# Optimization experiments

Measured on AMD Instinct MI355X. Metric: run time of the kernel, lower is better.

Reference implementation:

```python
import jax, jax.numpy as jnp
import numpy as np

N_NODES = 30000
N_EDGES = 480000
NFEAT = 256
HEADS = 4
C0 = 64      # layer0 out_channels
C1 = 40      # layer1 out_channels = nclass
NEG_SLOPE = 0.2
EPS = 1e-16


def glorot(key, shape, fan):
    # PyG glorot: uniform(-s, s), s = sqrt(6/(fan_in+fan_out)) over last 2 dims
    s = float(np.sqrt(6.0 / fan))
    return jax.random.uniform(key, shape, jnp.float32, -s, s)


def setup_inputs() -> dict:
    key = jax.random.key(0)
    ks = jax.random.split(key, 10)
    x = jax.random.normal(ks[0], (N_NODES, NFEAT), jnp.float32)
    src = jax.random.randint(ks[1], (N_EDGES,), 0, N_NODES)
    off = jax.random.randint(ks[2], (N_EDGES,), 1, N_NODES)
    dst = (src + off) % N_NODES  # guaranteed no self loops
    edge_index = jnp.stack([src, dst]).astype(jnp.int64)
    # layer 0 params (in=256 -> heads*out = 4*64, concat=True)
    w0 = glorot(ks[3], (NFEAT, HEADS * C0), NFEAT + HEADS * C0)
    att0 = glorot(ks[4], (1, HEADS, 2 * C0), HEADS + 2 * C0)
    b0 = jnp.zeros((HEADS * C0,), jnp.float32)
    # layer 1 params (in=256 -> heads*out = 4*40, concat=False)
    w1 = glorot(ks[5], (HEADS * C0, HEADS * C1), HEADS * C0 + HEADS * C1)
    att1 = glorot(ks[6], (1, HEADS, 2 * C1), HEADS + 2 * C1)
    b1 = jnp.zeros((C1,), jnp.float32)
    return {"x": x, "edge_index": edge_index, "w0": w0, "att0": att0,
            "b0": b0, "w1": w1, "att1": att1, "b1": b1}


def geo_layer(x, row, col, W, att, bias, heads, out_ch, concat):
    n = x.shape[0]
    h = (x @ W).reshape(n, heads, out_ch)          # [N,H,C]
    x_i = h[row]                                   # [E,H,C] gather (target per old-PyG i=0)
    x_j = h[col]                                   # [E,H,C]
    # 'gat' attention: leaky_relu(sum(cat(x_i,x_j) * att))
    a_l = att[:, :, :out_ch]
    a_r = att[:, :, out_ch:]
    alpha = jnp.sum(x_i * a_l, -1) + jnp.sum(x_j * a_r, -1)   # [E,H]
    alpha = jax.nn.leaky_relu(alpha, NEG_SLOPE)
    # segment softmax over target node (row)
    amax = jax.ops.segment_max(alpha, row, num_segments=n)
    ex = jnp.exp(alpha - amax[row])
    denom = jax.ops.segment_sum(ex, row, num_segments=n)
    alpha = ex / (denom[row] + EPS)
    neighbor = x_j * alpha[..., None]              # [E,H,C]
    out = jax.ops.segment_sum(neighbor, row, num_segments=n)  # [N,H,C]
    if concat:
        out = out.reshape(n, heads * out_ch)
    else:
        out = out.mean(axis=1)
    return out + bias


def reference(x, edge_index, w0, att0, b0, w1, att1, b1):
    n = x.shape[0]
    loops = jnp.arange(n, dtype=edge_index.dtype)
    row = jnp.concatenate([edge_index[0], loops])
    col = jnp.concatenate([edge_index[1], loops])
    out = geo_layer(x, row, col, w0, att0, b0, HEADS, C0, True)
    out = jax.nn.relu(out)
    out = geo_layer(out, row, col, w1, att1, b1, HEADS, C1, False)
    return out  # [N, nclass]
```

## Files before the change

### kernel.cpp

```cpp
#include <hip/hip_runtime.h>
#include <math.h>

#define N_NODES 30000
#define N_EDGESN 480000
#define NFEAT 256
#define HEADS 4
#define C0V 64
#define C1V 40
#define HC0 (HEADS*C0V)
#define HC1 (HEADS*C1V)
#define NEG_SLOPE 0.2f
#define EPSV 1e-16f

typedef unsigned short ushort_t;
typedef __attribute__((ext_vector_type(8))) short short8v;
typedef __attribute__((ext_vector_type(4))) float f32x4;

__device__ __forceinline__ float lrelu(float x) { return x >= 0.f ? x : x * NEG_SLOPE; }

__device__ __forceinline__ float b2f(unsigned int u16) {
  union { unsigned int u; float f; } v; v.u = u16 << 16; return v.f;
}
__device__ __forceinline__ float b2f_lo(unsigned int u) {
  union { unsigned int u; float f; } v; v.u = u << 16; return v.f;
}
__device__ __forceinline__ float b2f_hi(unsigned int u) {
  union { unsigned int u; float f; } v; v.u = u & 0xffff0000u; return v.f;
}
__device__ __forceinline__ unsigned short f2b(float f) {
  union { float f; unsigned int u; } v; v.f = f;
  unsigned int u = v.u + 0x7FFFu + ((v.u >> 16) & 1u);
  return (unsigned short)(u >> 16);
}

__global__ __launch_bounds__(256) void wtrans_both(const float* __restrict__ W0,
    const float* __restrict__ W1, ushort_t* __restrict__ W0t,
    ushort_t* __restrict__ W1t) {
  const int idx = blockIdx.x * 256 + threadIdx.x;
  constexpr int T0 = NFEAT * HC0;
  constexpr int T1 = HC0 * HC1;
  if (idx < T0) {
    const int k = idx / HC0, nf = idx - k * HC0;
    W0t[(size_t)nf * NFEAT + k] = f2b(W0[idx]);
  } else if (idx < T0 + T1) {
    const int i2 = idx - T0;
    const int k = i2 / HC1, nf = i2 - k * HC1;
    W1t[(size_t)nf * HC0 + k] = f2b(W1[i2]);
  }
}

#define KDIM 256
#define KPAD 264
template <int NFW, int CG, int NSTRIP, bool A_F32, int FUSE>
__global__ __launch_bounds__(256) void gemm_mfma2(const void* __restrict__ Ap,
    const ushort_t* __restrict__ Wt, ushort_t* __restrict__ C, int M,
    const float* __restrict__ att, float* __restrict__ al, float* __restrict__ ar) {
  __shared__ ushort_t As[NSTRIP][16][KPAD];
  const int tid = threadIdx.x;
  const int row_base = blockIdx.x * (NSTRIP * 16);
  constexpr int CHUNKS = NSTRIP * 16 * (KDIM / 8);
  for (int c = tid; c < CHUNKS; c += 256) {
    const int r = c / (KDIM / 8);
    const int ko = (c - r * (KDIM / 8)) * 8;
    const int s = r >> 4, rr = r & 15;
    uint4 w = make_uint4(0u, 0u, 0u, 0u);
    if (row_base + r < M) {
      if (A_F32) {
        const float* A = (const float*)Ap + (size_t)(row_base + r) * KDIM + ko;
        const float4 lo = *reinterpret_cast<const float4*>(A);
        const float4 hi = *reinterpret_cast<const float4*>(A + 4);
        w.x = (unsigned)f2b(lo.x) | ((unsigned)f2b(lo.y) << 16);
        w.y = (unsigned)f2b(lo.z) | ((unsigned)f2b(lo.w) << 16);
        w.z = (unsigned)f2b(hi.x) | ((unsigned)f2b(hi.y) << 16);
        w.w = (unsigned)f2b(hi.z) | ((unsigned)f2b(hi.w) << 16);
      } else {
        w = *reinterpret_cast<const uint4*>(
            (const ushort_t*)Ap + (size_t)(row_base + r) * KDIM + ko);
      }
    }
    *reinterpret_cast<uint4*>(&As[s][rr][ko]) = w;
  }
  __syncthreads();

  const int wid = tid >> 6, lane = tid & 63;
  const int s = wid / CG, cg = wid - s * CG;
  const int r_a = lane & 15, kg = lane >> 4;
  const int row0 = row_base + s * 16;
  constexpr int N = CG * NFW * 16;

  f32x4 acc[NFW];
#pragma unroll
  for (int f = 0; f < NFW; ++f) acc[f] = (f32x4){0.f, 0.f, 0.f, 0.f};

#pragma unroll
  for (int k0 = 0; k0 < KDIM; k0 += 32) {
    const short8v a = *reinterpret_cast<const short8v*>(&As[s][r_a][k0 + kg * 8]);
#pragma unroll
    for (int f = 0; f < NFW; ++f) {
      const short8v b = *reinterpret_cast<const short8v*>(
          Wt + (size_t)((cg * NFW + f) * 16 + r_a) * KDIM + k0 + kg * 8);
      acc[f] = __builtin_amdgcn_mfma_f32_16x16x32_bf16(a, b, acc[f], 0, 0, 0);
    }
  }
  if (row0 >= M) return;
#pragma unroll
  for (int f = 0; f < NFW; ++f) {
#pragma unroll
    for (int r = 0; r < 4; ++r) {
      C[(size_t)(row0 + kg * 4 + r) * N + (cg * NFW + f) * 16 + r_a] = f2b(acc[f][r]);
    }
  }
  if (FUSE == 1) {
    float hpl[4] = {0.f, 0.f, 0.f, 0.f}, hpr[4] = {0.f, 0.f, 0.f, 0.f};
#pragma unroll
    for (int f = 0; f < NFW; ++f) {
      const int cc = f * 16 + r_a;
      const float wlv = att[cg * 128 + cc];
      const float wrv = att[cg * 128 + 64 + cc];
#pragma unroll
      for (int r = 0; r < 4; ++r) {
        hpl[r] = fmaf(acc[f][r], wlv, hpl[r]);
        hpr[r] = fmaf(acc[f][r], wrv, hpr[r]);
      }
    }
#pragma unroll
    for (int o = 1; o < 16; o <<= 1) {
#pragma unroll
      for (int r = 0; r < 4; ++r) {
        hpl[r] += __shfl_xor(hpl[r], o);
        hpr[r] += __shfl_xor(hpr[r], o);
      }
    }
    if (r_a == 0) {
#pragma unroll
      for (int r = 0; r < 4; ++r) {
        const int row = row0 + kg * 4 + r;
        al[(size_t)row * 4 + cg] = hpl[r];
        ar[(size_t)row * 4 + cg] = hpr[r];
      }
    }
  } else if (FUSE == 2) {
    float hpa[4] = {0,0,0,0}, hpb[4] = {0,0,0,0};
    float hra[4] = {0,0,0,0}, hrb[4] = {0,0,0,0};
#pragma unroll
    for (int f = 0; f < NFW; ++f) {
      const int col = cg * 80 + f * 16 + r_a;
      const int hd = col / 40;
      const int cc = col - hd * 40;
      const float wlv = att[hd * 80 + cc];
      const float wrv = att[hd * 80 + 40 + cc];
      const bool isB = (hd & 1);
#pragma unroll
      for (int r = 0; r < 4; ++r) {
        const float v = acc[f][r];
        if (isB) { hpb[r] = fmaf(v, wlv, hpb[r]); hrb[r] = fmaf(v, wrv, hrb[r]); }
        else     { hpa[r] = fmaf(v, wlv, hpa[r]); hra[r] = fmaf(v, wrv, hra[r]); }
      }
    }
#pragma unroll
    for (int o = 1; o < 16; o <<= 1) {
#pragma unroll
      for (int r = 0; r < 4; ++r) {
        hpa[r] += __shfl_xor(hpa[r], o); hpb[r] += __shfl_xor(hpb[r], o);
        hra[r] += __shfl_xor(hra[r], o); hrb[r] += __shfl_xor(hrb[r], o);
      }
    }
    if (r_a == 0) {
#pragma unroll
      for (int r = 0; r < 4; ++r) {
        const int row = row0 + kg * 4 + r;
        al[(size_t)row * 4 + cg * 2 + 0] = hpa[r];
        al[(size_t)row * 4 + cg * 2 + 1] = hpb[r];
        ar[(size_t)row * 4 + cg * 2 + 0] = hra[r];
        ar[(size_t)row * 4 + cg * 2 + 1] = hrb[r];
      }
    }
  }
}

__global__ void hist_kernel(const int* __restrict__ src, int* __restrict__ deg, int E) {
  const int e = blockIdx.x * blockDim.x + threadIdx.x;
  if (e < E) atomicAdd(&deg[src[e]], 1);
}

__global__ __launch_bounds__(1024) void scan_kernel(const int* __restrict__ deg,
    int* __restrict__ rowstart, int n) {
  __shared__ int carry;
  __shared__ int wsum[16];
  const int tid = threadIdx.x;
  const int lane = tid & 63, w = tid >> 6;
  if (tid == 0) { carry = 0; rowstart[0] = 0; }
  __syncthreads();
  for (int base = 0; base < n; base += 1024) {
    const int idx = base + tid;
    int x = (idx < n) ? deg[idx] : 0;
#pragma unroll
    for (int o = 1; o < 64; o <<= 1) { int y = __shfl_up(x, o); if (lane >= o) x += y; }
    if (lane == 63) wsum[w] = x;
    __syncthreads();
    if (w == 0) {
      int s = (lane < 16) ? wsum[lane] : 0;
#pragma unroll
      for (int o = 1; o < 16; o <<= 1) { int y = __shfl_up(s, o); if (lane >= o) s += y; }
      if (lane < 16) wsum[lane] = s;
    }
    __syncthreads();
    const int add = (w > 0 ? wsum[w - 1] : 0) + carry;
    if (idx < n) rowstart[idx + 1] = x + add;
    __syncthreads();
    if (tid == 0) carry += wsum[15];
    __syncthreads();
  }
}

__global__ void scatter_kernel(const int* __restrict__ src, const int* __restrict__ dst,
    const int* __restrict__ rowstart, int* __restrict__ fill, int* __restrict__ scol,
    int E) {
  const int e = blockIdx.x * blockDim.x + threadIdx.x;
  if (e < E) {
    const int r = src[e];
    const int pos = rowstart[r] + atomicAdd(&fill[r], 1);
    scol[pos] = dst[e];
  }
}

template <int C, bool CONCAT_RELU>
__global__ __launch_bounds__(256) void gat_agg6(const ushort_t* __restrict__ h,
    const float* __restrict__ al, const float* __restrict__ ar,
    const int* __restrict__ rowstart, const int* __restrict__ scol,
    const float* __restrict__ bias, void* __restrict__ outv, int n) {
  constexpr int ROW = HEADS * C;
  constexpr int LPG = ROW / 8;
  constexpr int NG  = 64 / LPG;
  constexpr int EMAX = N_EDGESN - 1;
  __shared__ float smA[CONCAT_RELU ? 1 : 4][CONCAT_RELU ? 1 : NG]
                      [CONCAT_RELU ? 1 : ROW];
  __shared__ float smT[CONCAT_RELU ? 1 : 4][CONCAT_RELU ? 1 : NG * LPG];
  const int wid = threadIdx.x >> 6, lane = threadIdx.x & 63;
  const int i = blockIdx.x * 4 + wid;
  if (i >= n) return;
  const int s0 = rowstart[i], s1 = rowstart[i + 1];

  const float4 al4 = *reinterpret_cast<const float4*>(al + (size_t)i * 4);
  const float4 ari = *reinterpret_cast<const float4*>(ar + (size_t)i * 4);
  const float es0 = __expf(lrelu(al4.x + ari.x));
  const float es1 = __expf(lrelu(al4.y + ari.y));
  const float es2 = __expf(lrelu(al4.z + ari.z));
  const float es3 = __expf(lrelu(al4.w + ari.w));

  const int g  = lane / LPG;
  const int cl = lane - g * LPG;
  const bool act = g < NG;
  const int hd = (cl * 8) / C;
  const float al_h = hd < 2 ? (hd == 0 ? al4.x : al4.y) : (hd == 2 ? al4.z : al4.w);
  const float es_h = hd < 2 ? (hd == 0 ? es0 : es1) : (hd == 2 ? es2 : es3);

  float t = 0.f;
  float acc[8];
#pragma unroll
  for (int k = 0; k < 8; ++k) acc[k] = 0.f;

  if (g == 0) {
    const uint4 hv = *reinterpret_cast<const uint4*>(h + (size_t)i * ROW + cl * 8);
    acc[0] = es_h * b2f_lo(hv.x); acc[1] = es_h * b2f_hi(hv.x);
    acc[2] = es_h * b2f_lo(hv.y); acc[3] = es_h * b2f_hi(hv.y);
    acc[4] = es_h * b2f_lo(hv.z); acc[5] = es_h * b2f_hi(hv.z);
    acc[6] = es_h * b2f_lo(hv.w); acc[7] = es_h * b2f_hi(hv.w);
  }

#define FMA8(W, HV) \
  acc[0] = fmaf(W, b2f_lo(HV.x), acc[0]); acc[1] = fmaf(W, b2f_hi(HV.x), acc[1]); \
  acc[2] = fmaf(W, b2f_lo(HV.y), acc[2]); acc[3] = fmaf(W, b2f_hi(HV.y), acc[3]); \
  acc[4] = fmaf(W, b2f_lo(HV.z), acc[4]); acc[5] = fmaf(W, b2f_hi(HV.z), acc[5]); \
  acc[6] = fmaf(W, b2f_lo(HV.w), acc[6]); acc[7] = fmaf(W, b2f_hi(HV.w), acc[7])

  if (act) {
    int e = s0 + g;
    int ja = scol[min(e, EMAX)];
    int jb = scol[min(e + NG, EMAX)];
    for (; e + NG < s1; e += 2 * NG) {
      const int jc = scol[min(e + 2 * NG, EMAX)];
      const int jd = scol[min(e + 3 * NG, EMAX)];
      const float ara = ar[(size_t)ja * 4 + hd];
      const float arb = ar[(size_t)jb * 4 + hd];
      const uint4 ha = *reinterpret_cast<const uint4*>(h + (size_t)ja * ROW + cl * 8);
      const uint4 hb = *reinterpret_cast<const uint4*>(h + (size_t)jb * ROW + cl * 8);
      const float wa = __expf(lrelu(al_h + ara));
      const float wb = __expf(lrelu(al_h + arb));
      t += wa + wb;
      FMA8(wa, ha); FMA8(wb, hb);
      ja = jc; jb = jd;
    }
    if (e < s1) {
      const float ara = ar[(size_t)ja * 4 + hd];
      const uint4 ha = *reinterpret_cast<const uint4*>(h + (size_t)ja * ROW + cl * 8);
      const float wa = __expf(lrelu(al_h + ara));
      t += wa;
      FMA8(wa, ha);
    }
  }
#undef FMA8

  if (CONCAT_RELU) {
    t += __shfl_xor(t, 32);
    const float inv = 1.f / (t + es_h + EPSV);
#pragma unroll
    for (int k = 0; k < 8; ++k) acc[k] *= inv;
#pragma unroll
    for (int k = 0; k < 8; ++k) acc[k] += __shfl_xor(acc[k], 32);
    if (g == 0) {
      const float4 blo = *reinterpret_cast<const float4*>(bias + cl * 8);
      const float4 bhi = *reinterpret_cast<const float4*>(bias + cl * 8 + 4);
      uint4 st;
      st.x = (unsigned)f2b(fmaxf(acc[0] + blo.x, 0.f)) |
             ((unsigned)f2b(fmaxf(acc[1] + blo.y, 0.f)) << 16);
      st.y = (unsigned)f2b(fmaxf(acc[2] + blo.z, 0.f)) |
             ((unsigned)f2b(fmaxf(acc[3] + blo.w, 0.f)) << 16);
      st.z = (unsigned)f2b(fmaxf(acc[4] + bhi.x, 0.f)) |
             ((unsigned)f2b(fmaxf(acc[5] + bhi.y, 0.f)) << 16);
      st.w = (unsigned)f2b(fmaxf(acc[6] + bhi.z, 0.f)) |
             ((unsigned)f2b(fmaxf(acc[7] + bhi.w, 0.f)) << 16);
      *reinterpret_cast<uint4*>((ushort_t*)outv + (size_t)i * ROW + cl * 8) = st;
    }
  } else {
    if (act) {
#pragma unroll
      for (int k = 0; k < 8; ++k) smA[wid][g][cl * 8 + k] = acc[k];
      smT[wid][g * LPG + cl] = t;
    }
    __syncthreads();
    if (lane < C) {
      const float es[4] = {es0, es1, es2, es3};
      float s = 0.f;
#pragma unroll
      for (int hh = 0; hh < HEADS; ++hh) {
        float den = es[hh];
#pragma unroll
        for (int gg = 0; gg < NG; ++gg)
          den += smT[wid][gg * LPG + hh * 5];
        float chan = 0.f;
#pragma unroll
        for (int gg = 0; gg < NG; ++gg) chan += smA[wid][gg][hh * C + lane];
        s += chan / (den + EPSV);
      }
      ((float*)outv)[(size_t)i * C + lane] = s * 0.25f + bias[lane];
    }
  }
}

extern "C" void kernel_launch(void* const* d_in, const int* in_sizes, int n_in,
                              void* d_out, int out_size, void* d_ws, size_t ws_size,
                              hipStream_t stream) {
  const float* x    = (const float*)d_in[0];
  const int*   ei   = (const int*)d_in[1];
  const float* w0   = (const float*)d_in[2];
  const float* att0 = (const float*)d_in[3];
  const float* b0   = (const float*)d_in[4];
  const float* w1   = (const float*)d_in[5];
  const float* att1 = (const float*)d_in[6];
  const float* b1   = (const float*)d_in[7];
  float* out = (float*)d_out;

  char* ws = (char*)d_ws;
  size_t off = 0;
  auto alloc = [&](size_t bytes) -> void* {
    void* p = ws + off;
    off += (bytes + 255) & ~(size_t)255;
    return p;
  };
  ushort_t* h0b = (ushort_t*)alloc((size_t)N_NODES * HC0 * 2);
  ushort_t* o0b = (ushort_t*)alloc((size_t)N_NODES * HC0 * 2);
  float* al0 = (float*)alloc((size_t)N_NODES * HEADS * 4);
  float* ar0 = (float*)alloc((size_t)N_NODES * HEADS * 4);
  ushort_t* w0t = (ushort_t*)alloc((size_t)HC0 * NFEAT * 2);
  ushort_t* w1t = (ushort_t*)alloc((size_t)HC1 * HC0 * 2);
  int* deg      = (int*)alloc((size_t)N_NODES * 4);
  int* fill     = (int*)alloc((size_t)N_NODES * 4);
  int* rowstart = (int*)alloc((size_t)(N_NODES + 1) * 4);
  int* scol     = (int*)alloc((size_t)N_EDGESN * 4);
  ushort_t* h1b = h0b;
  float* al1 = al0;
  float* ar1 = ar0;

  const int* srcp = ei;
  const int* dstp = ei + N_EDGESN;

  const size_t zlen = (size_t)((char*)fill - (char*)deg) + (size_t)N_NODES * 4;
  hipMemsetAsync(deg, 0, zlen, stream);
  hist_kernel<<<(N_EDGESN + 255) / 256, 256, 0, stream>>>(srcp, deg, N_EDGESN);
  scan_kernel<<<1, 1024, 0, stream>>>(deg, rowstart, N_NODES);
  scatter_kernel<<<(N_EDGESN + 255) / 256, 256, 0, stream>>>(srcp, dstp, rowstart,
                                                             fill, scol, N_EDGESN);
  wtrans_both<<<(NFEAT * HC0 + HC0 * HC1 + 255) / 256, 256, 0, stream>>>(
      w0, w1, w0t, w1t);

  gemm_mfma2<4, 4, 1, true, 1><<<N_NODES / 16, 256, 0, stream>>>(
      x, w0t, h0b, N_NODES, att0, al0, ar0);
  gat_agg6<C0V, true><<<(N_NODES + 3) / 4, 256, 0, stream>>>(
      h0b, al0, ar0, rowstart, scol, b0, o0b, N_NODES);
  gemm_mfma2<5, 2, 2, false, 2><<<(N_NODES + 31) / 32, 256, 0, stream>>>(
      o0b, w1t, h1b, N_NODES, att1, al1, ar1);
  gat_agg6<C1V, false><<<(N_NODES + 3) / 4, 256, 0, stream>>>(
      h1b, al1, ar1, rowstart, scol, b1, out, N_NODES);
}
```

Baseline: 213.9 us.

## Make GEMMs persistent with register-resident weights and double-buffered A strips

Both dense projections become persistent kernels: each wave loads its slice of the transposed bf16 weight matrix into registers once, then loops over 16-row strips with a grid-stride step. The next strip's activations are prefetched into registers and written to a second LDS buffer while the current strip runs MFMAs, so global latency can overlap compute. The memset is replaced by a small zero kernel. The cost is much higher register pressure from holding weights (8×NFW short8 vectors per lane), which may reduce occupancy, plus fewer blocks per launch.

```diff
diff --git a/kernel.cpp b/kernel.cpp
--- a/kernel.cpp
+++ b/kernel.cpp
@@ -11,6 +11,8 @@
 #define HC1 (HEADS*C1V)
 #define NEG_SLOPE 0.2f
 #define EPSV 1e-16f
+#define KDIM 256
+#define KPAD 264
 
 typedef unsigned short ushort_t;
 typedef __attribute__((ext_vector_type(8))) short short8v;
@@ -18,9 +20,6 @@
 
 __device__ __forceinline__ float lrelu(float x) { return x >= 0.f ? x : x * NEG_SLOPE; }
 
-__device__ __forceinline__ float b2f(unsigned int u16) {
-  union { unsigned int u; float f; } v; v.u = u16 << 16; return v.f;
-}
 __device__ __forceinline__ float b2f_lo(unsigned int u) {
   union { unsigned int u; float f; } v; v.u = u << 16; return v.f;
 }
@@ -31,6 +30,11 @@
   union { float f; unsigned int u; } v; v.f = f;
   unsigned int u = v.u + 0x7FFFu + ((v.u >> 16) & 1u);
   return (unsigned short)(u >> 16);
+}
+
+__global__ __launch_bounds__(256) void zero_kernel(int* __restrict__ p, int n) {
+  const int i = blockIdx.x * 256 + threadIdx.x;
+  if (i < n) p[i] = 0;
 }
 
 __global__ __launch_bounds__(256) void wtrans_both(const float* __restrict__ W0,
@@ -49,133 +53,161 @@
   }
 }
 
-#define KDIM 256
-#define KPAD 264
-template <int NFW, int CG, int NSTRIP, bool A_F32, int FUSE>
-__global__ __launch_bounds__(256) void gemm_mfma2(const void* __restrict__ Ap,
-    const ushort_t* __restrict__ Wt, ushort_t* __restrict__ C, int M,
+template <int NFW, int CG, bool A_F32, int FUSE, int NT>
+__global__ __launch_bounds__(NT) void gemm_mfma3(const void* __restrict__ Ap,
+    const ushort_t* __restrict__ Wt, ushort_t* __restrict__ C, int nblk,
     const float* __restrict__ att, float* __restrict__ al, float* __restrict__ ar) {
-  __shared__ ushort_t As[NSTRIP][16][KPAD];
+  constexpr int S = N_NODES / 16;
+  constexpr int N = CG * NFW * 16;
+  constexpr int NCH = 16 * (KDIM / 8) / NT;
+  __shared__ ushort_t As[2][16][KPAD];
   const int tid = threadIdx.x;
-  const int row_base = blockIdx.x * (NSTRIP * 16);
-  constexpr int CHUNKS = NSTRIP * 16 * (KDIM / 8);
-  for (int c = tid; c < CHUNKS; c += 256) {
-    const int r = c / (KDIM / 8);
-    const int ko = (c - r * (KDIM / 8)) * 8;
-    const int s = r >> 4, rr = r & 15;
-    uint4 w = make_uint4(0u, 0u, 0u, 0u);
-    if (row_base + r < M) {
-      if (A_F32) {
-        const float* A = (const float*)Ap + (size_t)(row_base + r) * KDIM + ko;
-        const float4 lo = *reinterpret_cast<const float4*>(A);
-        const float4 hi = *reinterpret_cast<const float4*>(A + 4);
-        w.x = (unsigned)f2b(lo.x) | ((unsigned)f2b(lo.y) << 16);
-        w.y = (unsigned)f2b(lo.z) | ((unsigned)f2b(lo.w) << 16);
-        w.z = (unsigned)f2b(hi.x) | ((unsigned)f2b(hi.y) << 16);
-        w.w = (unsigned)f2b(hi.z) | ((unsigned)f2b(hi.w) << 16);
-      } else {
-        w = *reinterpret_cast<const uint4*>(
-            (const ushort_t*)Ap + (size_t)(row_base + r) * KDIM + ko);
-      }
-    }
-    *reinterpret_cast<uint4*>(&As[s][rr][ko]) = w;
+  const int lane = tid & 63, cg = tid >> 6;
+  const int r_a = lane & 15, kg = lane >> 4;
+
+  short8v B[8][NFW];
+#pragma unroll
+  for (int ks = 0; ks < 8; ++ks)
+#pragma unroll
+    for (int f = 0; f < NFW; ++f)
+      B[ks][f] = *reinterpret_cast<const short8v*>(
+          Wt + (size_t)((cg * NFW + f) * 16 + r_a) * KDIM + ks * 32 + kg * 8);
+
+#define STAGE_LOAD(STRIP, STG)                                                   \
+  _Pragma("unroll")                                                              \
+  for (int q = 0; q < NCH; ++q) {                                                \
+    const int c = tid + q * NT;                                                  \
+    const int r = c >> 5, ko = (c & 31) * 8;                                     \
+    if (A_F32) {                                                                 \
+      const float* A = (const float*)Ap + (size_t)((STRIP) * 16 + r) * KDIM + ko;\
+      const float4 lo = *reinterpret_cast<const float4*>(A);                     \
+      const float4 hi = *reinterpret_cast<const float4*>(A + 4);                 \
+      STG[q].x = (unsigned)f2b(lo.x) | ((unsigned)f2b(lo.y) << 16);              \
+      STG[q].y = (unsigned)f2b(lo.z) | ((unsigned)f2b(lo.w) << 16);              \
+      STG[q].z = (unsigned)f2b(hi.x) | ((unsigned)f2b(hi.y) << 16);              \
+      STG[q].w = (unsigned)f2b(hi.z) | ((unsigned)f2b(hi.w) << 16);              \
+    } else {                                                                     \
+      STG[q] = *reinterpret_cast<const uint4*>(                                  \
+          (const ushort_t*)Ap + (size_t)((STRIP) * 16 + r) * KDIM + ko);         \
+    }                                                                            \
+  }
+#define STAGE_WRITE(BUF, STG)                                                    \
+  _Pragma("unroll")                                                              \
+  for (int q = 0; q < NCH; ++q) {                                                \
+    const int c = tid + q * NT;                                                  \
+    const int r = c >> 5, ko = (c & 31) * 8;                                     \
+    *reinterpret_cast<uint4*>(&As[BUF][r][ko]) = STG[q];                         \
+  }
+
+  int strip = blockIdx.x;
+  {
+    uint4 stg[NCH];
+    STAGE_LOAD(strip, stg)
+    STAGE_WRITE(0, stg)
   }
   __syncthreads();
 
-  const int wid = tid >> 6, lane = tid & 63;
-  const int s = wid / CG, cg = wid - s * CG;
-  const int r_a = lane & 15, kg = lane >> 4;
-  const int row0 = row_base + s * 16;
-  constexpr int N = CG * NFW * 16;
-
-  f32x4 acc[NFW];
-#pragma unroll
-  for (int f = 0; f < NFW; ++f) acc[f] = (f32x4){0.f, 0.f, 0.f, 0.f};
-
-#pragma unroll
-  for (int k0 = 0; k0 < KDIM; k0 += 32) {
-    const short8v a = *reinterpret_cast<const short8v*>(&As[s][r_a][k0 + kg * 8]);
+  int buf = 0;
+  while (true) {
+    const int next = strip + nblk;
+    const bool has_next = next < S;
+    uint4 stg[NCH];
+    if (has_next) { STAGE_LOAD(next, stg) }
+
+    f32x4 acc[NFW];
+#pragma unroll
+    for (int f = 0; f < NFW; ++f) acc[f] = (f32x4){0.f, 0.f, 0.f, 0.f};
+#pragma unroll
+    for (int ks = 0; ks < 8; ++ks) {
+      const short8v a =
+          *reinterpret_cast<const short8v*>(&As[buf][r_a][ks * 32 + kg * 8]);
+#pragma unroll
+      for (int f = 0; f < NFW; ++f)
+        acc[f] = __builtin_amdgcn_mfma_f32_16x16x32_bf16(a, B[ks][f], acc[f], 0, 0, 0);
+    }
+    const int row0 = strip * 16;
 #pragma unroll
     for (int f = 0; f < NFW; ++f) {
-      const short8v b = *reinterpret_cast<const short8v*>(
-          Wt + (size_t)((cg * NFW + f) * 16 + r_a) * KDIM + k0 + kg * 8);
-      acc[f] = __builtin_amdgcn_mfma_f32_16x16x32_bf16(a, b, acc[f], 0, 0, 0);
-    }
-  }
-  if (row0 >= M) return;
-#pragma unroll
-  for (int f = 0; f < NFW; ++f) {
-#pragma unroll
-    for (int r = 0; r < 4; ++r) {
-      C[(size_t)(row0 + kg * 4 + r) * N + (cg * NFW + f) * 16 + r_a] = f2b(acc[f][r]);
-    }
-  }
-  if (FUSE == 1) {
-    float hpl[4] = {0.f, 0.f, 0.f, 0.f}, hpr[4] = {0.f, 0.f, 0.f, 0.f};
-#pragma unroll
-    for (int f = 0; f < NFW; ++f) {
-      const int cc = f * 16 + r_a;
-      const float wlv = att[cg * 128 + cc];
-      const float wrv = att[cg * 128 + 64 + cc];
 #pragma unroll
       for (int r = 0; r < 4; ++r) {
-        hpl[r] = fmaf(acc[f][r], wlv, hpl[r]);
-        hpr[r] = fmaf(acc[f][r], wrv, hpr[r]);
-      }
-    }
-#pragma unroll
-    for (int o = 1; o < 16; o <<= 1) {
-#pragma unroll
-      for (int r = 0; r < 4; ++r) {
-        hpl[r] += __shfl_xor(hpl[r], o);
-        hpr[r] += __shfl_xor(hpr[r], o);
-      }
-    }
-    if (r_a == 0) {
-#pragma unroll
-      for (int r = 0; r < 4; ++r) {
-        const int row = row0 + kg * 4 + r;
-        al[(size_t)row * 4 + cg] = hpl[r];
-        ar[(size_t)row * 4 + cg] = hpr[r];
-      }
-    }
-  } else if (FUSE == 2) {
-    float hpa[4] = {0,0,0,0}, hpb[4] = {0,0,0,0};
-    float hra[4] = {0,0,0,0}, hrb[4] = {0,0,0,0};
-#pragma unroll
-    for (int f = 0; f < NFW; ++f) {
-      const int col = cg * 80 + f * 16 + r_a;
-      const int hd = col / 40;
-      const int cc = col - hd * 40;
-      const float wlv = att[hd * 80 + cc];
-      const float wrv = att[hd * 80 + 40 + cc];
-      const bool isB = (hd & 1);
-#pragma unroll
-      for (int r = 0; r < 4; ++r) {
-        const float v = acc[f][r];
-        if (isB) { hpb[r] = fmaf(v, wlv, hpb[r]); hrb[r] = fmaf(v, wrv, hrb[r]); }
-        else     { hpa[r] = fmaf(v, wlv, hpa[r]); hra[r] = fmaf(v, wrv, hra[r]); }
-      }
-    }
-#pragma unroll
-    for (int o = 1; o < 16; o <<= 1) {
-#pragma unroll
-      for (int r = 0; r < 4; ++r) {
-        hpa[r] += __shfl_xor(hpa[r], o); hpb[r] += __shfl_xor(hpb[r], o);
-        hra[r] += __shfl_xor(hra[r], o); hrb[r] += __shfl_xor(hrb[r], o);
-      }
-    }
-    if (r_a == 0) {
-#pragma unroll
-      for (int r = 0; r < 4; ++r) {
-        const int row = row0 + kg * 4 + r;
-        al[(size_t)row * 4 + cg * 2 + 0] = hpa[r];
-        al[(size_t)row * 4 + cg * 2 + 1] = hpb[r];
-        ar[(size_t)row * 4 + cg * 2 + 0] = hra[r];
-        ar[(size_t)row * 4 + cg * 2 + 1] = hrb[r];
-      }
-    }
-  }
+        C[(size_t)(row0 + kg * 4 + r) * N + (cg * NFW + f) * 16 + r_a] =
+            f2b(acc[f][r]);
+      }
+    }
+    if (FUSE == 1) {
+      float hpl[4] = {0.f, 0.f, 0.f, 0.f}, hpr[4] = {0.f, 0.f, 0.f, 0.f};
+#pragma unroll
+      for (int f = 0; f < NFW; ++f) {
+        const int cc = f * 16 + r_a;
+        const float wlv = att[cg * 128 + cc];
+        const float wrv = att[cg * 128 + 64 + cc];
+#pragma unroll
+        for (int r = 0; r < 4; ++r) {
+          hpl[r] = fmaf(acc[f][r], wlv, hpl[r]);
+          hpr[r] = fmaf(acc[f][r], wrv, hpr[r]);
+        }
+      }
+#pragma unroll
+      for (int o = 1; o < 16; o <<= 1) {
+#pragma unroll
+        for (int r = 0; r < 4; ++r) {
+          hpl[r] += __shfl_xor(hpl[r], o);
+          hpr[r] += __shfl_xor(hpr[r], o);
+        }
+      }
+      if (r_a == 0) {
+#pragma unroll
+        for (int r = 0; r < 4; ++r) {
+          const int row = row0 + kg * 4 + r;
+          al[(size_t)row * 4 + cg] = hpl[r];
+          ar[(size_t)row * 4 + cg] = hpr[r];
+        }
+      }
+    } else if (FUSE == 2) {
+      float hpa[4] = {0,0,0,0}, hpb[4] = {0,0,0,0};
+      float hra[4] = {0,0,0,0}, hrb[4] = {0,0,0,0};
+#pragma unroll
+      for (int f = 0; f < NFW; ++f) {
+        const int col = cg * 80 + f * 16 + r_a;
+        const int hd = col / 40;
+        const int cc = col - hd * 40;
+        const float wlv = att[hd * 80 + cc];
+        const float wrv = att[hd * 80 + 40 + cc];
+        const bool isB = (hd & 1);
+#pragma unroll
+        for (int r = 0; r < 4; ++r) {
+          const float v = acc[f][r];
+          if (isB) { hpb[r] = fmaf(v, wlv, hpb[r]); hrb[r] = fmaf(v, wrv, hrb[r]); }
+          else     { hpa[r] = fmaf(v, wlv, hpa[r]); hra[r] = fmaf(v, wrv, hra[r]); }
+        }
+      }
+#pragma unroll
+      for (int o = 1; o < 16; o <<= 1) {
+#pragma unroll
+        for (int r = 0; r < 4; ++r) {
+          hpa[r] += __shfl_xor(hpa[r], o); hpb[r] += __shfl_xor(hpb[r], o);
+          hra[r] += __shfl_xor(hra[r], o); hrb[r] += __shfl_xor(hrb[r], o);
+        }
+      }
+      if (r_a == 0) {
+#pragma unroll
+        for (int r = 0; r < 4; ++r) {
+          const int row = row0 + kg * 4 + r;
+          al[(size_t)row * 4 + cg * 2 + 0] = hpa[r];
+          al[(size_t)row * 4 + cg * 2 + 1] = hpb[r];
+          ar[(size_t)row * 4 + cg * 2 + 0] = hra[r];
+          ar[(size_t)row * 4 + cg * 2 + 1] = hrb[r];
+        }
+      }
+    }
+
+    if (!has_next) break;
+    STAGE_WRITE(buf ^ 1, stg)
+    __syncthreads();
+    strip = next; buf ^= 1;
+  }
+#undef STAGE_LOAD
+#undef STAGE_WRITE
 }
 
 __global__ void hist_kernel(const int* __restrict__ src, int* __restrict__ deg, int E) {
@@ -385,8 +417,8 @@
   const int* srcp = ei;
   const int* dstp = ei + N_EDGESN;
 
-  const size_t zlen = (size_t)((char*)fill - (char*)deg) + (size_t)N_NODES * 4;
-  hipMemsetAsync(deg, 0, zlen, stream);
+  const int ztot = (int)(fill - deg) + N_NODES;
+  zero_kernel<<<(ztot + 255) / 256, 256, 0, stream>>>(deg, ztot);
   hist_kernel<<<(N_EDGESN + 255) / 256, 256, 0, stream>>>(srcp, deg, N_EDGESN);
   scan_kernel<<<1, 1024, 0, stream>>>(deg, rowstart, N_NODES);
   scatter_kernel<<<(N_EDGESN + 255) / 256, 256, 0, stream>>>(srcp, dstp, rowstart,
@@ -394,12 +426,12 @@
   wtrans_both<<<(NFEAT * HC0 + HC0 * HC1 + 255) / 256, 256, 0, stream>>>(
       w0, w1, w0t, w1t);
 
-  gemm_mfma2<4, 4, 1, true, 1><<<N_NODES / 16, 256, 0, stream>>>(
-      x, w0t, h0b, N_NODES, att0, al0, ar0);
+  gemm_mfma3<4, 4, true, 1, 256><<<625, 256, 0, stream>>>(
+      x, w0t, h0b, 625, att0, al0, ar0);
   gat_agg6<C0V, true><<<(N_NODES + 3) / 4, 256, 0, stream>>>(
       h0b, al0, ar0, rowstart, scol, b0, o0b, N_NODES);
-  gemm_mfma2<5, 2, 2, false, 2><<<(N_NODES + 31) / 32, 256, 0, stream>>>(
-      o0b, w1t, h1b, N_NODES, att1, al1, ar1);
+  gemm_mfma3<5, 2, false, 2, 128><<<938, 128, 0, stream>>>(
+      o0b, w1t, h1b, 938, att1, al1, ar1);
   gat_agg6<C1V, false><<<(N_NODES + 3) / 4, 256, 0, stream>>>(
       h1b, al1, ar1, rowstart, scol, b1, out, N_NODES);
 }
```

Measured after the change: 196.9 us. -7.9%, faster.
